# Kernel optimization log

Hardware: AMD Instinct MI355X
Metric: run time of the kernel (lower is better)

Reference implementation:

```python
import jax, jax.numpy as jnp
import numpy as np
from jax import lax

B = 2048      # batch
EMB = 128     # embedding_size
NF = 200      # num_filters
NR = 10000    # num_roles
NV = 50000    # num_values
ARITY = 5
EPS = 1e-5    # BatchNorm eps (torch default)


def setup_inputs() -> dict:
    key = jax.random.key(0)
    ks = jax.random.split(key, 12)
    bound = float(np.sqrt(1.0 / EMB))
    emb_roles = jax.random.uniform(ks[0], (NR, EMB), jnp.float32, -bound, bound).at[0].set(0.0)
    emb_values = jax.random.uniform(ks[1], (NV, EMB), jnp.float32, -bound, bound).at[0].set(0.0)
    D = NF * (EMB - 2)
    return {
        "x_batch": jax.random.randint(ks[2], (B, 2 * ARITY), 0, 10000),
        "arity": ARITY,
        "mode": 0,
        "emb_roles": emb_roles,
        "emb_values": emb_values,
        "conv1_w": jax.random.normal(ks[3], (NF, 1, 3, 3), jnp.float32) * 0.1,
        "conv1_b": jnp.zeros((NF,), jnp.float32),
        "bn1_gamma": jnp.ones((NF,), jnp.float32),
        "bn1_beta": jnp.zeros((NF,), jnp.float32),
        "conv2_w": jax.random.normal(ks[4], (NF, 1, 5, 3), jnp.float32) * 0.1,
        "conv2_b": jnp.zeros((NF,), jnp.float32),
        "bn2_gamma": jnp.ones((NF,), jnp.float32),
        "bn2_beta": jnp.zeros((NF,), jnp.float32),
        "fc_w": jax.random.normal(ks[5], (1, D), jnp.float32) * float(np.sqrt(2.0 / (D + 1))),
        "fc_b": jnp.zeros((1,), jnp.float32),
    }


def _conv(x, w, b):
    # x: [N,1,H,E], w: [F,1,kh,3] -> [N,F,1,E-2] (VALID conv; kh == H)
    y = lax.conv_general_dilated(x, w, (1, 1), 'VALID',
                                 dimension_numbers=('NCHW', 'OIHW', 'NCHW'))
    return y + b[None, :, None, None]


def reference(x_batch, arity, mode, emb_roles, emb_values,
              conv1_w, conv1_b, bn1_gamma, bn1_beta,
              conv2_w, conv2_b, bn2_gamma, bn2_beta, fc_w, fc_b):
    n = x_batch.shape[0]
    roles = x_batch[:, 0::2]
    vals = x_batch[:, 1::2]
    fr = emb_roles[roles[:, :2]]    # [B,2,E]
    fv = emb_values[vals[:, :2]]    # [B,2,E]
    # (head_value, role, tail_value) rows -> [B,3,E]
    hrt = jnp.stack([fv[:, 0], fr[:, 0], fv[:, 1]], axis=1)

    # primary triple branch: conv1 + BatchNorm (batch stats) + ReLU
    y1 = _conv(hrt[:, None], conv1_w, conv1_b)[:, :, 0, :]   # [B,F,E-2]
    m1 = y1.mean(axis=(0, 2), keepdims=True)
    v1 = y1.var(axis=(0, 2), keepdims=True)
    y1 = jax.nn.relu((y1 - m1) * jax.lax.rsqrt(v1 + EPS)
                     * bn1_gamma[None, :, None] + bn1_beta[None, :, None])
    feats = y1.reshape(n, -1)[:, None, :]                    # [B,1,D]

    if arity > 2:
        k = arity - 2
        kr = emb_roles[roles[:, 2:]]   # [B,K,E]
        kv = emb_values[vals[:, 2:]]   # [B,K,E]
        e = hrt.shape[-1]
        hrt_b = jnp.broadcast_to(hrt[:, None], (n, k, 3, e))
        x2 = jnp.concatenate([hrt_b, kr[:, :, None, :], kv[:, :, None, :]], axis=2)  # [B,K,5,E]
        y2 = _conv(x2.reshape(n * k, 1, 5, e), conv2_w, conv2_b)[:, :, 0, :]
        y2 = y2.reshape(n, k, y2.shape[1], y2.shape[2])      # [B,K,F,E-2]
        # original loop batch-norms each kv slot independently -> stats over (batch, width) per slot
        m2 = y2.mean(axis=(0, 3), keepdims=True)
        v2 = y2.var(axis=(0, 3), keepdims=True)
        y2 = jax.nn.relu((y2 - m2) * jax.lax.rsqrt(v2 + EPS)
                         * bn2_gamma[None, None, :, None] + bn2_beta[None, None, :, None])
        feats = jnp.concatenate([feats, y2.reshape(n, k, -1)], axis=1)  # [B,arity-1,D]

    min_val = feats.min(axis=1)                              # [B,D]
    return min_val @ fc_w.T + fc_b                           # [B,1]
```

## Files before the change

### kernel.cpp

```cpp
#include <hip/hip_runtime.h>

#define BB 2048
#define EMB 128
#define NF 200
#define W_OUT 126
#define EPS 1e-5f

#define NCOPY 8
#define FCWQ_BYTE_OFF 32768
#define FCWQ_HALFS (50 * 2 * 64 * 4)
#define AWF_BYTE_OFF 83968
#define WS_NEED (AWF_BYTE_OFF + 50 * 64 * 8 * 2)
#define AWF_FALLBACK_OFF 4096
#define WS_FALLBACK_NEED (AWF_FALLBACK_OFF + 50 * 64 * 8 * 2)

#define SPBS 4
#define STATS_BLOCKS (BB / SPBS)
#define SPBM 2
#define MAIN_BLOCKS (BB / SPBM)

typedef _Float16 half8 __attribute__((ext_vector_type(8)));
typedef _Float16 half4v __attribute__((ext_vector_type(4)));
typedef float f32x4v __attribute__((ext_vector_type(4)));

__device__ __forceinline__ const float* rowptr(const int* __restrict__ xr, int r,
                                               const float* __restrict__ er,
                                               const float* __restrict__ ev) {
  if (r == 0) return ev + (size_t)xr[1] * EMB;
  if (r == 1) return er + (size_t)xr[0] * EMB;
  if (r == 2) return ev + (size_t)xr[3] * EMB;
  const int k = (r - 3) >> 1;
  return ((r - 3) & 1) ? ev + (size_t)xr[5 + 2 * k] * EMB
                       : er + (size_t)xr[4 + 2 * k] * EMB;
}

__global__ __launch_bounds__(256, 2) void stats_mfma(
    const int* __restrict__ xb, const float* __restrict__ er,
    const float* __restrict__ ev, float* __restrict__ gout, int ncop,
    const float* __restrict__ fcw, _Float16* __restrict__ fcwQh, int do_swz) {
  __shared__ _Float16 Bt[SPBS][40][136];
  __shared__ float Gred[SPBS][1024];
  const int tid = threadIdx.x;
  const int base = blockIdx.x * SPBS;

  if (do_swz && blockIdx.x < (FCWQ_HALFS + 255) / 256) {
    const int idx = blockIdx.x * 256 + tid;
    if (idx < FCWQ_HALFS) {
      const int mtile = idx >> 9;
      const int rem = idx & 511;
      const int jh = rem >> 8;
      const int rem2 = rem & 255;
      const int l = rem2 >> 2;
      const int j = rem2 & 3;
      const int f = mtile * 4 + (l >> 4);
      const int x = (jh * 4 + j) * 16 + (l & 15);
      fcwQh[idx] = (_Float16)((x < W_OUT) ? fcw[(size_t)f * W_OUT + x] : 0.f);
    }
  }

  for (int job = tid; job < SPBS * 136; job += 256) {
    const int s = job / 136, x = job % 136;
    if (x < W_OUT) {
      const int* xr = xb + (size_t)(base + s) * 10;
#pragma unroll
      for (int r = 0; r < 9; r++) {
        const float* hp = rowptr(xr, r, er, ev);
        Bt[s][3 * r + 0][x] = (_Float16)hp[x];
        Bt[s][3 * r + 1][x] = (_Float16)hp[x + 1];
        Bt[s][3 * r + 2][x] = (_Float16)hp[x + 2];
      }
      Bt[s][27][x] = (_Float16)1.0f;
#pragma unroll
      for (int k = 28; k < 40; k++) Bt[s][k][x] = (_Float16)0.f;
    } else {
#pragma unroll
      for (int k = 0; k < 40; k++) Bt[s][k][x] = (_Float16)0.f;
    }
  }
  __syncthreads();

  const int w = tid >> 6, l = tid & 63;
  const int tl = l & 15, kl = l >> 4;
  f32x4v a00 = {0.f, 0.f, 0.f, 0.f}, a01 = a00, a10 = a00, a11 = a00;
#pragma unroll
  for (int c = 0; c < 4; c++) {
    const int x0 = c * 32 + kl * 8;
    const half8 g0 = *(const half8*)&Bt[w][tl][x0];
    const half8 g1 = *(const half8*)&Bt[w][16 + tl][x0];
    a00 = __builtin_amdgcn_mfma_f32_16x16x32_f16(g0, g0, a00, 0, 0, 0);
    a01 = __builtin_amdgcn_mfma_f32_16x16x32_f16(g0, g1, a01, 0, 0, 0);
    a10 = __builtin_amdgcn_mfma_f32_16x16x32_f16(g1, g0, a10, 0, 0, 0);
    a11 = __builtin_amdgcn_mfma_f32_16x16x32_f16(g1, g1, a11, 0, 0, 0);
  }
#pragma unroll
  for (int r = 0; r < 4; r++) {
    const int rm = kl * 4 + r;
    Gred[w][rm * 32 + tl]             = a00[r];
    Gred[w][rm * 32 + 16 + tl]        = a01[r];
    Gred[w][(16 + rm) * 32 + tl]      = a10[r];
    Gred[w][(16 + rm) * 32 + 16 + tl] = a11[r];
  }
  __syncthreads();
  float* gslice = gout + (blockIdx.x & (ncop - 1)) * 1024;
  for (int idx = tid; idx < 1024; idx += 256) {
    float s = Gred[0][idx] + Gred[1][idx] + Gred[2][idx] + Gred[3][idx];
    atomicAdd(&gslice[idx], s);
  }
}

__global__ __launch_bounds__(256) void finalize_kernel(
    const float* __restrict__ w1, const float* __restrict__ w2,
    const float* __restrict__ g1, const float* __restrict__ be1,
    const float* __restrict__ g2, const float* __restrict__ be2,
    const float* __restrict__ gbuf, _Float16* __restrict__ AwF, int ncop) {
  __shared__ float G[1024];
  const int tid = threadIdx.x;
  for (int e = tid; e < 1024; e += 256) {
    float v = 0.f;
    for (int c = 0; c < ncop; c++) v += gbuf[c * 1024 + e];
    G[e] = v;
  }
  __syncthreads();
  const int f = tid;
  if (f >= NF) return;
  float w1r[9], w2r[15];
#pragma unroll
  for (int j = 0; j < 9; j++)  w1r[j] = w1[f * 9 + j];
#pragma unroll
  for (int j = 0; j < 15; j++) w2r[j] = w2[f * 15 + j];
  const float invN = 1.0f / (float)(BB * W_OUT);
  const int m = f >> 2, q4 = (f & 3) * 4;

  float m1 = 0.f, q1 = 0.f;
#pragma unroll
  for (int i = 0; i < 9; i++) {
    m1 = fmaf(w1r[i], G[i * 32 + 27], m1);
#pragma unroll
    for (int j = 0; j < 9; j++) q1 = fmaf(w1r[i] * w1r[j], G[i * 32 + j], q1);
  }
  m1 *= invN;
  float v1 = q1 * invN - m1 * m1;
  float sc1 = g1[f] * rsqrtf(v1 + EPS);
  float sh1 = be1[f] - m1 * sc1;
  {
    float row[32];
#pragma unroll
    for (int k = 0; k < 32; k++) row[k] = 0.f;
#pragma unroll
    for (int i = 0; i < 9; i++) row[i] = w1r[i] * sc1;
    row[27] = sh1;
#pragma unroll
    for (int g = 0; g < 4; g++) {
      half8 h;
#pragma unroll
      for (int e = 0; e < 8; e++) h[e] = (_Float16)row[g * 8 + e];
      *(half8*)&AwF[(size_t)(m * 64 + g * 16 + q4 + 0) * 8] = h;
    }
  }

  float mcm = 0.f, qc = 0.f;
#pragma unroll
  for (int i = 0; i < 9; i++) {
    mcm = fmaf(w2r[i], G[i * 32 + 27], mcm);
#pragma unroll
    for (int j = 0; j < 9; j++) qc = fmaf(w2r[i] * w2r[j], G[i * 32 + j], qc);
  }
#pragma unroll
  for (int kk = 0; kk < 3; kk++) {
    const int a = 3 + 2 * kk, b = 4 + 2 * kk;
    float m2 = mcm, cross = 0.f, qa = 0.f, qb = 0.f, qab = 0.f;
#pragma unroll
    for (int j = 0; j < 3; j++) {
      m2 = fmaf(w2r[9 + j],  G[(3 * a + j) * 32 + 27], m2);
      m2 = fmaf(w2r[12 + j], G[(3 * b + j) * 32 + 27], m2);
    }
#pragma unroll
    for (int i = 0; i < 9; i++) {
      float t = 0.f;
#pragma unroll
      for (int j = 0; j < 3; j++) {
        t = fmaf(w2r[9 + j],  G[i * 32 + 3 * a + j], t);
        t = fmaf(w2r[12 + j], G[i * 32 + 3 * b + j], t);
      }
      cross = fmaf(w2r[i], t, cross);
    }
#pragma unroll
    for (int j = 0; j < 3; j++)
#pragma unroll
      for (int jp = 0; jp < 3; jp++) {
        qa  = fmaf(w2r[9 + j]  * w2r[9 + jp],  G[(3 * a + j) * 32 + 3 * a + jp], qa);
        qb  = fmaf(w2r[12 + j] * w2r[12 + jp], G[(3 * b + j) * 32 + 3 * b + jp], qb);
        qab = fmaf(w2r[9 + j]  * w2r[12 + jp], G[(3 * a + j) * 32 + 3 * b + jp], qab);
      }
    float q2 = qc + 2.f * cross + qa + qb + 2.f * qab;
    float mean2 = m2 * invN;
    float v2 = q2 * invN - mean2 * mean2;
    float sck = g2[f] * rsqrtf(v2 + EPS);
    float shk = be2[f] - mean2 * sck;

    float row[32];
#pragma unroll
    for (int k = 0; k < 32; k++) row[k] = 0.f;
#pragma unroll
    for (int i = 0; i < 9; i++) row[i] = w2r[i] * sck;
#pragma unroll
    for (int j = 0; j < 3; j++) {
      row[3 * a + j] = w2r[9 + j]  * sck;
      row[3 * b + j] = w2r[12 + j] * sck;
    }
    row[27] = shk;
#pragma unroll
    for (int g = 0; g < 4; g++) {
      half8 h;
#pragma unroll
      for (int e = 0; e < 8; e++) h[e] = (_Float16)row[g * 8 + e];
      *(half8*)&AwF[(size_t)(m * 64 + g * 16 + q4 + 1 + kk) * 8] = h;
    }
  }
}

template <bool SWZ>
__global__ __launch_bounds__(256, 2) void main_mfma(
    const int* __restrict__ xb, const float* __restrict__ er,
    const float* __restrict__ ev, const float* __restrict__ fcw,
    const _Float16* __restrict__ fcwQh, const _Float16* __restrict__ AwF,
    const float* __restrict__ fcb, float* __restrict__ out) {
  __shared__ _Float16 AfL[50 * 64 * 8];
  __shared__ _Float16 Bm[SPBM][128][40];
  __shared__ float red[4];
  const int tid = threadIdx.x;
  const int base = blockIdx.x * SPBM;

  {
    const uint2* __restrict__ Ag = (const uint2*)AwF;
    uint2* Al = (uint2*)AfL;
#pragma unroll
    for (int i = 0; i < 25; ++i) Al[tid + i * 256] = Ag[tid + i * 256];
  }
  {
    const int s = tid >> 7, x = tid & 127;
    const int* xr = xb + (size_t)(base + s) * 10;
    const int x1 = (x + 1 < 128) ? x + 1 : 127;
    const int x2 = (x + 2 < 128) ? x + 2 : 127;
    _Float16* dst = &Bm[s][x][0];
#pragma unroll
    for (int r = 0; r < 9; r++) {
      const float* hp = rowptr(xr, r, er, ev);
      dst[3 * r + 0] = (_Float16)hp[x];
      dst[3 * r + 1] = (_Float16)hp[x1];
      dst[3 * r + 2] = (_Float16)hp[x2];
    }
    dst[27] = (_Float16)1.0f;
#pragma unroll
    for (int k = 28; k < 40; k++) dst[k] = (_Float16)0.f;
  }
  __syncthreads();

  const int w = tid >> 6, l = tid & 63;
  const int sW = w >> 1, mh = w & 1;
  const int xl = l & 15, fl = l >> 4;
  const float fcb0 = fcb[0];

  float psum = 0.f;
#pragma unroll 1
  for (int jh = 0; jh < 2; ++jh) {
    half8 bf[4];
#pragma unroll
    for (int j = 0; j < 4; ++j)
      bf[j] = *(const half8*)&Bm[sW][(jh * 4 + j) * 16 + xl][fl * 8];
#pragma unroll 1
    for (int mtb = 0; mtb < 5; ++mtb) {
      half8 af[5];
#pragma unroll
      for (int i = 0; i < 5; ++i) {
        const int mtile = mh * 25 + mtb * 5 + i;
        af[i] = *(const half8*)&AfL[(size_t)(mtile * 64 + l) * 8];
      }
#pragma unroll
      for (int i = 0; i < 5; ++i) {
        const int mtile = mh * 25 + mtb * 5 + i;
        const int fo = mtile * 4 + fl;
        half4v fqh;
        if (SWZ)
          fqh = *(const half4v*)&fcwQh[((size_t)(mtile * 2 + jh) * 64 + l) * 4];
#pragma unroll
        for (int j = 0; j < 4; ++j) {
          f32x4v acc = __builtin_amdgcn_mfma_f32_16x16x32_f16(
              af[i], bf[j], (f32x4v){0.f, 0.f, 0.f, 0.f}, 0, 0, 0);
          float fcv;
          if (SWZ) {
            fcv = (float)fqh[j];
          } else {
            const int x = (jh * 4 + j) * 16 + xl;
            const bool xv = (x < W_OUT);
            const float fcl = fcw[(size_t)fo * W_OUT + (xv ? x : 0)];
            fcv = xv ? fcl : 0.f;
          }
          float mv = fminf(fminf(fminf(acc[0], acc[1]), acc[2]), acc[3]);
          psum = fmaf(fmaxf(mv, 0.f), fcv, psum);
        }
      }
    }
  }

#pragma unroll
  for (int off = 32; off; off >>= 1) psum += __shfl_xor(psum, off, 64);
  if (l == 0) red[w] = psum;
  __syncthreads();
  if (tid < SPBM)
    out[base + tid] = red[2 * tid] + red[2 * tid + 1] + fcb0;
}

extern "C" void kernel_launch(void* const* d_in, const int* in_sizes, int n_in,
                              void* d_out, int out_size, void* d_ws, size_t ws_size,
                              hipStream_t stream) {
  const int* xb    = (const int*)d_in[0];
  const float* er  = (const float*)d_in[3];
  const float* ev  = (const float*)d_in[4];
  const float* w1  = (const float*)d_in[5];
  const float* g1  = (const float*)d_in[7];
  const float* be1 = (const float*)d_in[8];
  const float* w2  = (const float*)d_in[9];
  const float* g2  = (const float*)d_in[11];
  const float* be2 = (const float*)d_in[12];
  const float* fcw = (const float*)d_in[13];
  const float* fcb = (const float*)d_in[14];
  float* ws  = (float*)d_ws;
  float* out = (float*)d_out;

  const int full = (ws_size >= (size_t)WS_NEED) ? 1 : 0;
  float* gbuf = ws;
  _Float16* fcwQh = (_Float16*)((char*)d_ws + FCWQ_BYTE_OFF);
  _Float16* AwF = (_Float16*)((char*)d_ws +
                              (full ? AWF_BYTE_OFF : AWF_FALLBACK_OFF));
  const int ncop = full ? NCOPY : 1;

  hipMemsetAsync(gbuf, 0, (size_t)ncop * 1024 * sizeof(float), stream);
  hipLaunchKernelGGL(stats_mfma, dim3(STATS_BLOCKS), dim3(256), 0, stream,
                     xb, er, ev, gbuf, ncop, fcw, fcwQh, full);
  hipLaunchKernelGGL(finalize_kernel, dim3(1), dim3(256), 0, stream,
                     w1, w2, g1, be1, g2, be2, gbuf, AwF, ncop);
  if (full)
    hipLaunchKernelGGL((main_mfma<true>), dim3(MAIN_BLOCKS), dim3(256), 0,
                       stream, xb, er, ev, fcw, fcwQh, AwF, fcb, out);
  else
    hipLaunchKernelGGL((main_mfma<false>), dim3(MAIN_BLOCKS), dim3(256), 0,
                       stream, xb, er, ev, fcw, fcwQh, AwF, fcb, out);
}
```

Measured before the change: 47.42 us.

## Fuse finalize into stats via last-block counter; process four samples per main block

The separate single-block finalize kernel is folded into the stats kernel. A global atomic counter elects the last finishing block, which reduces the Gram copies and builds the BN-folded weights, so one launch and its gap are removed. The main kernel now handles four samples per block in two pairs, so the 100KB weight tile loaded into shared memory is reused across twice as many samples. The second pair's embeddings are prefetched into registers while the first pair computes. The costs are a serialized tail on the last stats block, extra register pressure from the 27-float prefetch buffer, and half as many main blocks.

```diff
diff --git a/kernel.cpp b/kernel.cpp
--- a/kernel.cpp
+++ b/kernel.cpp
@@ -7,17 +7,18 @@
 #define EPS 1e-5f
 
 #define NCOPY 8
-#define FCWQ_BYTE_OFF 32768
+#define G_BYTES 32768
+#define CNT_OFF_B 32768
+#define FCWQ_OFF_B 33024
 #define FCWQ_HALFS (50 * 2 * 64 * 4)
-#define AWF_BYTE_OFF 83968
-#define WS_NEED (AWF_BYTE_OFF + 50 * 64 * 8 * 2)
-#define AWF_FALLBACK_OFF 4096
-#define WS_FALLBACK_NEED (AWF_FALLBACK_OFF + 50 * 64 * 8 * 2)
+#define AWF_OFF_B 84224
+#define WS_NEED (AWF_OFF_B + 50 * 64 * 8 * 2)
+#define FB_CNT_OFF_B 4096
+#define FB_AWF_OFF_B 4608
 
 #define SPBS 4
 #define STATS_BLOCKS (BB / SPBS)
-#define SPBM 2
-#define MAIN_BLOCKS (BB / SPBM)
+#define MAIN_BLOCKS (BB / 4)
 
 typedef _Float16 half8 __attribute__((ext_vector_type(8)));
 typedef _Float16 half4v __attribute__((ext_vector_type(4)));
@@ -37,9 +38,15 @@
 __global__ __launch_bounds__(256, 2) void stats_mfma(
     const int* __restrict__ xb, const float* __restrict__ er,
     const float* __restrict__ ev, float* __restrict__ gout, int ncop,
-    const float* __restrict__ fcw, _Float16* __restrict__ fcwQh, int do_swz) {
+    const float* __restrict__ fcw, _Float16* __restrict__ fcwQh, int do_swz,
+    unsigned int* __restrict__ cnt,
+    const float* __restrict__ w1, const float* __restrict__ w2,
+    const float* __restrict__ g1, const float* __restrict__ be1,
+    const float* __restrict__ g2, const float* __restrict__ be2,
+    _Float16* __restrict__ AwF) {
   __shared__ _Float16 Bt[SPBS][40][136];
   __shared__ float Gred[SPBS][1024];
+  __shared__ int lastFlag;
   const int tid = threadIdx.x;
   const int base = blockIdx.x * SPBS;
 
@@ -86,11 +93,11 @@
   for (int c = 0; c < 4; c++) {
     const int x0 = c * 32 + kl * 8;
     const half8 g0 = *(const half8*)&Bt[w][tl][x0];
-    const half8 g1 = *(const half8*)&Bt[w][16 + tl][x0];
+    const half8 g1v = *(const half8*)&Bt[w][16 + tl][x0];
     a00 = __builtin_amdgcn_mfma_f32_16x16x32_f16(g0, g0, a00, 0, 0, 0);
-    a01 = __builtin_amdgcn_mfma_f32_16x16x32_f16(g0, g1, a01, 0, 0, 0);
-    a10 = __builtin_amdgcn_mfma_f32_16x16x32_f16(g1, g0, a10, 0, 0, 0);
-    a11 = __builtin_amdgcn_mfma_f32_16x16x32_f16(g1, g1, a11, 0, 0, 0);
+    a01 = __builtin_amdgcn_mfma_f32_16x16x32_f16(g0, g1v, a01, 0, 0, 0);
+    a10 = __builtin_amdgcn_mfma_f32_16x16x32_f16(g1v, g0, a10, 0, 0, 0);
+    a11 = __builtin_amdgcn_mfma_f32_16x16x32_f16(g1v, g1v, a11, 0, 0, 0);
   }
 #pragma unroll
   for (int r = 0; r < 4; r++) {
@@ -106,18 +113,23 @@
     float s = Gred[0][idx] + Gred[1][idx] + Gred[2][idx] + Gred[3][idx];
     atomicAdd(&gslice[idx], s);
   }
-}
-
-__global__ __launch_bounds__(256) void finalize_kernel(
-    const float* __restrict__ w1, const float* __restrict__ w2,
-    const float* __restrict__ g1, const float* __restrict__ be1,
-    const float* __restrict__ g2, const float* __restrict__ be2,
-    const float* __restrict__ gbuf, _Float16* __restrict__ AwF, int ncop) {
-  __shared__ float G[1024];
-  const int tid = threadIdx.x;
+
+  __syncthreads();
+  if (tid == 0) {
+    __threadfence();
+    unsigned old = atomicAdd(cnt, 1u);
+    lastFlag = (old == (unsigned)(gridDim.x - 1)) ? 1 : 0;
+  }
+  __syncthreads();
+  if (!lastFlag) return;
+  __threadfence();
+
+  float* G = &Gred[0][0];
   for (int e = tid; e < 1024; e += 256) {
     float v = 0.f;
-    for (int c = 0; c < ncop; c++) v += gbuf[c * 1024 + e];
+    for (int c = 0; c < ncop; c++)
+      v += __hip_atomic_load(&gout[c * 1024 + e], __ATOMIC_RELAXED,
+                             __HIP_MEMORY_SCOPE_AGENT);
     G[e] = v;
   }
   __syncthreads();
@@ -226,10 +238,10 @@
     const _Float16* __restrict__ fcwQh, const _Float16* __restrict__ AwF,
     const float* __restrict__ fcb, float* __restrict__ out) {
   __shared__ _Float16 AfL[50 * 64 * 8];
-  __shared__ _Float16 Bm[SPBM][128][40];
+  __shared__ _Float16 Bm[2][128][40];
   __shared__ float red[4];
   const int tid = threadIdx.x;
-  const int base = blockIdx.x * SPBM;
+  const int base = blockIdx.x * 4;
 
   {
     const uint2* __restrict__ Ag = (const uint2*)AwF;
@@ -237,22 +249,35 @@
 #pragma unroll
     for (int i = 0; i < 25; ++i) Al[tid + i * 256] = Ag[tid + i * 256];
   }
-  {
-    const int s = tid >> 7, x = tid & 127;
-    const int* xr = xb + (size_t)(base + s) * 10;
-    const int x1 = (x + 1 < 128) ? x + 1 : 127;
-    const int x2 = (x + 2 < 128) ? x + 2 : 127;
-    _Float16* dst = &Bm[s][x][0];
+
+  const int sT = tid >> 7, xT = tid & 127;
+  const int x1 = (xT + 1 < 128) ? xT + 1 : 127;
+  const int x2 = (xT + 2 < 128) ? xT + 2 : 127;
+
+  {
+    const int* xr = xb + (size_t)(base + sT) * 10;
+    _Float16* dst = &Bm[sT][xT][0];
 #pragma unroll
     for (int r = 0; r < 9; r++) {
       const float* hp = rowptr(xr, r, er, ev);
-      dst[3 * r + 0] = (_Float16)hp[x];
+      dst[3 * r + 0] = (_Float16)hp[xT];
       dst[3 * r + 1] = (_Float16)hp[x1];
       dst[3 * r + 2] = (_Float16)hp[x2];
     }
     dst[27] = (_Float16)1.0f;
 #pragma unroll
     for (int k = 28; k < 40; k++) dst[k] = (_Float16)0.f;
+  }
+  float v1[27];
+  {
+    const int* xr = xb + (size_t)(base + 2 + sT) * 10;
+#pragma unroll
+    for (int r = 0; r < 9; r++) {
+      const float* hp = rowptr(xr, r, er, ev);
+      v1[3 * r + 0] = hp[xT];
+      v1[3 * r + 1] = hp[x1];
+      v1[3 * r + 2] = hp[x2];
+    }
   }
   __syncthreads();
 
@@ -261,54 +286,73 @@
   const int xl = l & 15, fl = l >> 4;
   const float fcb0 = fcb[0];
 
-  float psum = 0.f;
-#pragma unroll 1
-  for (int jh = 0; jh < 2; ++jh) {
-    half8 bf[4];
-#pragma unroll
-    for (int j = 0; j < 4; ++j)
-      bf[j] = *(const half8*)&Bm[sW][(jh * 4 + j) * 16 + xl][fl * 8];
-#pragma unroll 1
-    for (int mtb = 0; mtb < 5; ++mtb) {
-      half8 af[5];
-#pragma unroll
-      for (int i = 0; i < 5; ++i) {
-        const int mtile = mh * 25 + mtb * 5 + i;
-        af[i] = *(const half8*)&AfL[(size_t)(mtile * 64 + l) * 8];
-      }
-#pragma unroll
-      for (int i = 0; i < 5; ++i) {
-        const int mtile = mh * 25 + mtb * 5 + i;
-        const int fo = mtile * 4 + fl;
-        half4v fqh;
-        if (SWZ)
-          fqh = *(const half4v*)&fcwQh[((size_t)(mtile * 2 + jh) * 64 + l) * 4];
-#pragma unroll
-        for (int j = 0; j < 4; ++j) {
-          f32x4v acc = __builtin_amdgcn_mfma_f32_16x16x32_f16(
-              af[i], bf[j], (f32x4v){0.f, 0.f, 0.f, 0.f}, 0, 0, 0);
-          float fcv;
-          if (SWZ) {
-            fcv = (float)fqh[j];
-          } else {
-            const int x = (jh * 4 + j) * 16 + xl;
-            const bool xv = (x < W_OUT);
-            const float fcl = fcw[(size_t)fo * W_OUT + (xv ? x : 0)];
-            fcv = xv ? fcl : 0.f;
-          }
-          float mv = fminf(fminf(fminf(acc[0], acc[1]), acc[2]), acc[3]);
-          psum = fmaf(fmaxf(mv, 0.f), fcv, psum);
-        }
-      }
-    }
-  }
-
-#pragma unroll
-  for (int off = 32; off; off >>= 1) psum += __shfl_xor(psum, off, 64);
-  if (l == 0) red[w] = psum;
-  __syncthreads();
-  if (tid < SPBM)
-    out[base + tid] = red[2 * tid] + red[2 * tid + 1] + fcb0;
+#define COMPUTE_PAIR(PPIDX)                                                   \
+  {                                                                           \
+    float psum = 0.f;                                                         \
+    _Pragma("unroll 1")                                                       \
+    for (int jh = 0; jh < 2; ++jh) {                                          \
+      half8 bf[4];                                                            \
+      _Pragma("unroll")                                                       \
+      for (int j = 0; j < 4; ++j)                                             \
+        bf[j] = *(const half8*)&Bm[sW][(jh * 4 + j) * 16 + xl][fl * 8];       \
+      _Pragma("unroll 1")                                                     \
+      for (int mtb = 0; mtb < 5; ++mtb) {                                     \
+        half8 af[5];                                                          \
+        _Pragma("unroll")                                                     \
+        for (int i = 0; i < 5; ++i) {                                         \
+          const int mtile = mh * 25 + mtb * 5 + i;                            \
+          af[i] = *(const half8*)&AfL[(size_t)(mtile * 64 + l) * 8];          \
+        }                                                                     \
+        _Pragma("unroll")                                                     \
+        for (int i = 0; i < 5; ++i) {                                         \
+          const int mtile = mh * 25 + mtb * 5 + i;                            \
+          const int fo = mtile * 4 + fl;                                      \
+          half4v fqh;                                                         \
+          if (SWZ)                                                            \
+            fqh = *(const half4v*)&fcwQh[((size_t)(mtile * 2 + jh) * 64 + l) * 4]; \
+          _Pragma("unroll")                                                   \
+          for (int j = 0; j < 4; ++j) {                                       \
+            f32x4v acc = __builtin_amdgcn_mfma_f32_16x16x32_f16(              \
+                af[i], bf[j], (f32x4v){0.f, 0.f, 0.f, 0.f}, 0, 0, 0);         \
+            float fcv;                                                        \
+            if (SWZ) {                                                        \
+              fcv = (float)fqh[j];                                            \
+            } else {                                                          \
+              const int x = (jh * 4 + j) * 16 + xl;                           \
+              const bool xv = (x < W_OUT);                                    \
+              const float fcl = fcw[(size_t)fo * W_OUT + (xv ? x : 0)];       \
+              fcv = xv ? fcl : 0.f;                                           \
+            }                                                                 \
+            float mv = fminf(fminf(fminf(acc[0], acc[1]), acc[2]), acc[3]);   \
+            psum = fmaf(fmaxf(mv, 0.f), fcv, psum);                           \
+          }                                                                   \
+        }                                                                     \
+      }                                                                       \
+    }                                                                         \
+    _Pragma("unroll")                                                         \
+    for (int off = 32; off; off >>= 1) psum += __shfl_xor(psum, off, 64);     \
+    if (l == 0) red[w] = psum;                                                \
+    __syncthreads();                                                          \
+    if (tid < 2)                                                              \
+      out[base + 2 * (PPIDX) + tid] = red[2 * tid] + red[2 * tid + 1] + fcb0; \
+  }
+
+  COMPUTE_PAIR(0)
+  {
+    _Float16* dst = &Bm[sT][xT][0];
+#pragma unroll
+    for (int r = 0; r < 9; r++) {
+      dst[3 * r + 0] = (_Float16)v1[3 * r + 0];
+      dst[3 * r + 1] = (_Float16)v1[3 * r + 1];
+      dst[3 * r + 2] = (_Float16)v1[3 * r + 2];
+    }
+    dst[27] = (_Float16)1.0f;
+#pragma unroll
+    for (int k = 28; k < 40; k++) dst[k] = (_Float16)0.f;
+  }
+  __syncthreads();
+  COMPUTE_PAIR(1)
+#undef COMPUTE_PAIR
 }
 
 extern "C" void kernel_launch(void* const* d_in, const int* in_sizes, int n_in,
@@ -330,16 +374,18 @@
 
   const int full = (ws_size >= (size_t)WS_NEED) ? 1 : 0;
   float* gbuf = ws;
-  _Float16* fcwQh = (_Float16*)((char*)d_ws + FCWQ_BYTE_OFF);
+  unsigned int* cnt = (unsigned int*)((char*)d_ws +
+                                      (full ? CNT_OFF_B : FB_CNT_OFF_B));
+  _Float16* fcwQh = (_Float16*)((char*)d_ws + FCWQ_OFF_B);
   _Float16* AwF = (_Float16*)((char*)d_ws +
-                              (full ? AWF_BYTE_OFF : AWF_FALLBACK_OFF));
+                              (full ? AWF_OFF_B : FB_AWF_OFF_B));
   const int ncop = full ? NCOPY : 1;
 
-  hipMemsetAsync(gbuf, 0, (size_t)ncop * 1024 * sizeof(float), stream);
+  hipMemsetAsync(gbuf, 0,
+                 (size_t)(full ? (CNT_OFF_B + 4) : (FB_CNT_OFF_B + 4)), stream);
   hipLaunchKernelGGL(stats_mfma, dim3(STATS_BLOCKS), dim3(256), 0, stream,
-                     xb, er, ev, gbuf, ncop, fcw, fcwQh, full);
-  hipLaunchKernelGGL(finalize_kernel, dim3(1), dim3(256), 0, stream,
-                     w1, w2, g1, be1, g2, be2, gbuf, AwF, ncop);
+                     xb, er, ev, gbuf, ncop, fcw, fcwQh, full, cnt,
+                     w1, w2, g1, be1, g2, be2, AwF);
   if (full)
     hipLaunchKernelGGL((main_mfma<true>), dim3(MAIN_BLOCKS), dim3(256), 0,
                        stream, xb, er, ev, fcw, fcwQh, AwF, fcb, out);
```

After: 55.25 us. 1.17x slower.
